# Performance work log

Hardware: AMD Instinct MI355X
Metric: run time of the kernel (lower is better)

The kernel has to match this reference:

```python
import jax, jax.numpy as jnp
import numpy as np

N_NODES = 50000
N_EDGES = 800000
N_GRAPHS = 256
IN_DIM, HIDDEN_DIM, EMBED_DIM = 128, 64, 128


def setup_inputs() -> dict:
    key = jax.random.key(0)
    ks = jax.random.split(key, 8)
    x = jax.random.normal(ks[0], (N_NODES, IN_DIM), dtype=jnp.float32)
    edge_index = jax.random.randint(ks[1], (2, N_EDGES), 0, N_NODES, dtype=jnp.int64)
    edge_weight = jax.random.uniform(ks[2], (N_EDGES,), dtype=jnp.float32)
    batch_vec = jnp.sort(jax.random.randint(ks[3], (N_NODES,), 0, N_GRAPHS, dtype=jnp.int64))
    # Glorot-ish params for the two GCNConv layers
    W1 = jax.random.normal(ks[4], (IN_DIM, HIDDEN_DIM), dtype=jnp.float32) / np.sqrt(IN_DIM)
    b1 = jnp.zeros((HIDDEN_DIM,), dtype=jnp.float32)
    W2 = jax.random.normal(ks[5], (HIDDEN_DIM, EMBED_DIM), dtype=jnp.float32) / np.sqrt(HIDDEN_DIM)
    b2 = jnp.zeros((EMBED_DIM,), dtype=jnp.float32)
    return {"x": x, "edge_index": edge_index, "edge_weight": edge_weight,
            "batch_vec": batch_vec, "W1": W1, "b1": b1, "W2": W2, "b2": b2}


def _gcn_conv(x, src, dst, ew, W, b, num_nodes):
    # PyG GCNConv: linear transform, add self-loops (weight 1), sym-normalize, aggregate at dst.
    h = x @ W  # [N, out]
    loops = jnp.arange(num_nodes, dtype=src.dtype)
    row = jnp.concatenate([src, loops])
    col = jnp.concatenate([dst, loops])
    w = jnp.concatenate([ew, jnp.ones((num_nodes,), x.dtype)])
    deg = jax.ops.segment_sum(w, col, num_segments=num_nodes)
    dis = jnp.where(deg > 0, jax.lax.rsqrt(deg), 0.0)  # deg^{-1/2}, inf -> 0
    norm = dis[row] * w * dis[col]  # [E+N]
    msg = h[row] * norm[:, None]  # gather + scale
    out = jax.ops.segment_sum(msg, col, num_segments=num_nodes)  # scatter-add
    return out + b


def reference(x, edge_index, edge_weight, batch_vec, W1, b1, W2, b2):
    src, dst = edge_index[0], edge_index[1]
    h = jax.nn.relu(_gcn_conv(x, src, dst, edge_weight, W1, b1, N_NODES))
    # dropout is identity at inference
    h = jax.nn.relu(_gcn_conv(h, src, dst, edge_weight, W2, b2, N_NODES))
    # global_mean_pool over graphs
    s = jax.ops.segment_sum(h, batch_vec, num_segments=N_GRAPHS)
    cnt = jax.ops.segment_sum(jnp.ones((N_NODES,), h.dtype), batch_vec, num_segments=N_GRAPHS)
    return s / jnp.maximum(cnt, 1.0)[:, None]
```

## Files before the change

### kernel.cpp

```cpp
#include <hip/hip_runtime.h>

constexpr int N_NODES  = 50000;
constexpr int N_EDGES  = 800000;
constexpr int N_GRAPHS = 256;
constexpr int IN_DIM   = 128;
constexpr int HID      = 64;
constexpr int EMB      = 128;
constexpr int NBKT     = 391;
constexpr int BCAP     = 4096;
constexpr int EB       = (N_EDGES + 1023) / 1024;
constexpr int GB       = (N_NODES + 31) / 32;
constexpr int GSB      = (N_NODES + 255) / 256;
constexpr int NB2      = 64;

constexpr size_t OFF_POOL = 0;
constexpr size_t OFF_GCUR = 32768;
constexpr size_t OFF_GST  = 33160;
constexpr size_t OFF_DIS  = 33424;
constexpr size_t OFF_RS   = 83424;
constexpr size_t OFF_REC  = 133424;
constexpr size_t OFF_PART = OFF_REC + 2 * (size_t)NBKT * BCAP;
constexpr size_t OFF_H1   = OFF_PART;
constexpr size_t OFF_H1P  = OFF_PART + 4 * (size_t)NBKT * BCAP;
constexpr size_t OFF_AGG2 = OFF_H1P;

__device__ inline unsigned bf16r(float f) {
    unsigned u = __float_as_uint(f);
    return (u + 0x7fffu + ((u >> 16) & 1u)) >> 16;
}
__device__ inline unsigned bf16pack2(float lo, float hi) {
    return bf16r(lo) | (bf16r(hi) << 16);
}
__device__ inline float bflo(unsigned v) { return __uint_as_float(v << 16); }
__device__ inline float bfhi(unsigned v) { return __uint_as_float(v & 0xffff0000u); }

__device__ inline void fma4(float4& acc, float s, const float4& v) {
    acc.x += s * v.x; acc.y += s * v.y; acc.z += s * v.z; acc.w += s * v.w;
}

__global__ __launch_bounds__(256) void k_p2(const int* __restrict__ src,
                                            const int* __restrict__ dst,
                                            const float* __restrict__ ew,
                                            int* __restrict__ gcur,
                                            uint4* __restrict__ part,
                                            const int* __restrict__ batch,
                                            int* __restrict__ gstart) {
    __shared__ int   lb[NBKT];
    __shared__ int   lc[NBKT];
    __shared__ int   es[1024];
    __shared__ int   ed[1024];
    __shared__ float ee[1024];
    int tid = threadIdx.x;
    if (blockIdx.x >= EB) {
        int i = (blockIdx.x - EB) * 256 + tid;
        if (i >= N_NODES) return;
        int g = batch[i];
        if (i == 0) {
            for (int gg = 0; gg <= g; ++gg) gstart[gg] = 0;
        } else {
            int gp = batch[i - 1];
            for (int gg = gp + 1; gg <= g; ++gg) gstart[gg] = i;
        }
        if (i == N_NODES - 1) {
            for (int gg = g + 1; gg <= N_GRAPHS; ++gg) gstart[gg] = N_NODES;
        }
        return;
    }
    for (int i = tid; i < NBKT; i += 256) lc[i] = 0;
    __syncthreads();
    int base = blockIdx.x * 1024;
    #pragma unroll
    for (int j = 0; j < 4; ++j) {
        int idx = j * 256 + tid;
        int e = base + idx;
        int d = 0, s = 0; float w = 0.f;
        if (e < N_EDGES) {
            d = dst[e]; s = src[e]; w = ew[e];
            atomicAdd(&lc[d >> 7], 1);
        }
        es[idx] = s; ed[idx] = d; ee[idx] = w;
    }
    __syncthreads();
    for (int i = tid; i < NBKT; i += 256) {
        int c = lc[i];
        lb[i] = c ? (i * BCAP + atomicAdd(&gcur[i], c)) : 0;
        lc[i] = 0;
    }
    __syncthreads();
    #pragma unroll
    for (int j = 0; j < 4; ++j) {
        int idx = j * 256 + tid;
        int e = base + idx;
        if (e < N_EDGES) {
            int d = ed[idx];
            int b = d >> 7;
            int r = atomicAdd(&lc[b], 1);
            part[lb[b] + r] = make_uint4((unsigned)es[idx], (unsigned)d,
                                         __float_as_uint(ee[idx]), 0u);
        }
    }
}

constexpr int SMEM_BYTES = 32768 + 32 * (IN_DIM + 4) * 4;
__global__ __launch_bounds__(256) void k_p3_gemm1(const uint4* __restrict__ part,
                                                  const int* __restrict__ gcur,
                                                  int* __restrict__ rs,
                                                  float* __restrict__ dis,
                                                  uint2* __restrict__ rec,
                                                  const float* __restrict__ x,
                                                  const float* __restrict__ W1,
                                                  unsigned* __restrict__ h) {
    __shared__ alignas(16) unsigned char smem[SMEM_BYTES];
    int tid = threadIdx.x;
    if (blockIdx.x < NBKT) {
        uint2* cache = (uint2*)smem;
        int*   cnt   = (int*)(smem + 32768);
        float* dgw   = (float*)(smem + 32768 + 512);
        int*   scn   = (int*)(smem + 32768 + 1024);
        int*   curx  = (int*)(smem + 32768 + 1536);
        int b = blockIdx.x;
        int ebeg = b * BCAP;
        int ne = gcur[b]; if (ne > BCAP) ne = BCAP;
        if (tid < 128) { cnt[tid] = 0; dgw[tid] = 0.f; }
        __syncthreads();
        for (int i = tid; i < ne; i += 256) {
            uint4 r = part[ebeg + i];
            int ld = (int)r.y & 127;
            cache[i] = make_uint2(r.x | ((unsigned)ld << 16), r.z);
            atomicAdd(&cnt[ld], 1);
            atomicAdd(&dgw[ld], __uint_as_float(r.z));
        }
        __syncthreads();
        int c = (tid < 128) ? cnt[tid] : 0;
        if (tid < 128) scn[tid] = c;
        __syncthreads();
        for (int off = 1; off < 128; off <<= 1) {
            int a = (tid >= off && tid < 128) ? scn[tid - off] : 0;
            __syncthreads();
            if (tid < 128) scn[tid] += a;
            __syncthreads();
        }
        if (tid < 128) {
            int node = (b << 7) + tid;
            if (node < N_NODES) {
                rs[node] = ebeg + scn[tid];
                dis[node] = rsqrtf(dgw[tid] + 1.0f);
            }
            curx[tid] = ebeg + scn[tid] - c;
        }
        __syncthreads();
        for (int i = tid; i < ne; i += 256) {
            uint2 q = cache[i];
            int ld = (int)(q.x >> 16);
            int pos = atomicAdd(&curx[ld], 1);
            rec[pos] = make_uint2(q.x & 0xFFFFu, q.y);
        }
        return;
    }
    float* Ws = (float*)smem;
    float (*xs)[IN_DIM + 4] = (float (*)[IN_DIM + 4])(smem + 32768);
    int bid = blockIdx.x - NBKT;
    const float4* W4 = (const float4*)W1;
    float4* Ws4 = (float4*)Ws;
    for (int i = tid; i < IN_DIM * HID / 4; i += 256) Ws4[i] = W4[i];
    int base = bid * 32;
    const float4* X4 = (const float4*)x;
    for (int i = tid; i < 32 * 32; i += 256) {
        int ln = i >> 5, kq = i & 31;
        int node = base + ln;
        float4 v = (node < N_NODES) ? X4[(size_t)node * 32 + kq]
                                    : make_float4(0.f, 0.f, 0.f, 0.f);
        *(float4*)&xs[ln][kq * 4] = v;
    }
    __syncthreads();
    int np = tid >> 4;
    int q  = tid & 15;
    int n0 = np * 2, n1 = n0 + 1;
    float4 a0 = make_float4(0.f, 0.f, 0.f, 0.f);
    float4 a1 = a0;
    #pragma unroll 4
    for (int k4 = 0; k4 < IN_DIM; k4 += 4) {
        float4 xv0 = *(const float4*)&xs[n0][k4];
        float4 xv1 = *(const float4*)&xs[n1][k4];
        float4 w0 = Ws4[(k4 + 0) * 16 + q];
        float4 w1 = Ws4[(k4 + 1) * 16 + q];
        float4 w2 = Ws4[(k4 + 2) * 16 + q];
        float4 w3 = Ws4[(k4 + 3) * 16 + q];
        fma4(a0, xv0.x, w0); fma4(a0, xv0.y, w1); fma4(a0, xv0.z, w2); fma4(a0, xv0.w, w3);
        fma4(a1, xv1.x, w0); fma4(a1, xv1.y, w1); fma4(a1, xv1.z, w2); fma4(a1, xv1.w, w3);
    }
    int nd0 = base + n0, nd1 = base + n1;
    if (nd0 < N_NODES) {
        uint2 p = make_uint2(bf16pack2(a0.x, a0.y), bf16pack2(a0.z, a0.w));
        ((uint2*)h)[(size_t)nd0 * 16 + q] = p;
    }
    if (nd1 < N_NODES) {
        uint2 p = make_uint2(bf16pack2(a1.x, a1.y), bf16pack2(a1.z, a1.w));
        ((uint2*)h)[(size_t)nd1 * 16 + q] = p;
    }
}

template <bool RELU_BIAS, bool OUT_BF16>
__global__ __launch_bounds__(256) void k_gather64(const uint2* __restrict__ rec,
                                                  const int* __restrict__ rs,
                                                  const float* __restrict__ dis,
                                                  const unsigned* __restrict__ T,
                                                  const float* __restrict__ bias,
                                                  void* __restrict__ outv) {
    int wave = (blockIdx.x * 256 + threadIdx.x) >> 6;
    if (wave >= N_NODES) return;
    int lane = threadIdx.x & 63;
    int grp  = lane >> 4;
    int l    = lane & 15;
    int n = wave;
    int begin = ((n & 127) == 0) ? ((n >> 7) * BCAP) : rs[n - 1];
    int end = rs[n];
    const uint2* T2 = (const uint2*)T;

    float a0 = 0.f, a1 = 0.f, a2 = 0.f, a3 = 0.f;
    float c0 = 0.f, c1 = 0.f, c2 = 0.f, c3 = 0.f;
    int k = begin + grp;
    while (k + 4 < end) {
        uint2 r0 = rec[k];
        uint2 r1 = rec[k + 4];
        float d0 = dis[r0.x];
        float d1 = dis[r1.x];
        uint2 t0 = T2[(size_t)r0.x * 16 + l];
        uint2 t1 = T2[(size_t)r1.x * 16 + l];
        float n0 = d0 * __uint_as_float(r0.y);
        float n1 = d1 * __uint_as_float(r1.y);
        a0 += bflo(t0.x) * n0; a1 += bfhi(t0.x) * n0;
        a2 += bflo(t0.y) * n0; a3 += bfhi(t0.y) * n0;
        c0 += bflo(t1.x) * n1; c1 += bfhi(t1.x) * n1;
        c2 += bflo(t1.y) * n1; c3 += bfhi(t1.y) * n1;
        k += 8;
    }
    if (k < end) {
        uint2 r = rec[k];
        float d = dis[r.x];
        uint2 t = T2[(size_t)r.x * 16 + l];
        float nn = d * __uint_as_float(r.y);
        a0 += bflo(t.x) * nn; a1 += bfhi(t.x) * nn;
        a2 += bflo(t.y) * nn; a3 += bfhi(t.y) * nn;
    }
    a0 += c0; a1 += c1; a2 += c2; a3 += c3;
    a0 += __shfl_xor(a0, 16, 64); a1 += __shfl_xor(a1, 16, 64);
    a2 += __shfl_xor(a2, 16, 64); a3 += __shfl_xor(a3, 16, 64);
    a0 += __shfl_xor(a0, 32, 64); a1 += __shfl_xor(a1, 32, 64);
    a2 += __shfl_xor(a2, 32, 64); a3 += __shfl_xor(a3, 32, 64);
    if (grp == 0) {
        float di = dis[n];
        uint2 t = T2[(size_t)n * 16 + l];
        a0 += bflo(t.x) * di; a1 += bfhi(t.x) * di;
        a2 += bflo(t.y) * di; a3 += bfhi(t.y) * di;
        a0 *= di; a1 *= di; a2 *= di; a3 *= di;
        if (RELU_BIAS) {
            float4 b = ((const float4*)bias)[l];
            a0 = fmaxf(a0 + b.x, 0.f);
            a1 = fmaxf(a1 + b.y, 0.f);
            a2 = fmaxf(a2 + b.z, 0.f);
            a3 = fmaxf(a3 + b.w, 0.f);
        }
        if (OUT_BF16) {
            ((uint2*)outv)[(size_t)n * 16 + l] =
                make_uint2(bf16pack2(a0, a1), bf16pack2(a2, a3));
        } else {
            ((float4*)outv)[(size_t)n * 16 + l] = make_float4(a0, a1, a2, a3);
        }
    }
}

__global__ __launch_bounds__(256) void k_gemm2_pool(const float* __restrict__ agg,
                                                    const float* __restrict__ W2,
                                                    const float* __restrict__ b2,
                                                    const int* __restrict__ batch,
                                                    float* __restrict__ pool) {
    __shared__ float Ws[HID * EMB];
    __shared__ float as[NB2][HID];
    __shared__ int   bs[NB2];
    int tid = threadIdx.x;
    const float4* W4 = (const float4*)W2;
    float4* Ws4 = (float4*)Ws;
    for (int i = tid; i < HID * EMB / 4; i += 256) Ws4[i] = W4[i];
    int base = blockIdx.x * NB2;
    const float4* A4 = (const float4*)agg;
    float4* as4 = (float4*)as;
    for (int i = tid; i < NB2 * HID / 4; i += 256) {
        int node = base + (i >> 4);
        as4[i] = (node < N_NODES) ? A4[(size_t)node * 16 + (i & 15)]
                                  : make_float4(0.f, 0.f, 0.f, 0.f);
    }
    if (tid < NB2) {
        int node = base + tid;
        bs[tid] = (node < N_NODES) ? batch[node] : -1;
    }
    __syncthreads();

    int c = tid & 31;
    int s = tid >> 5;
    int jc = c * 4;
    int nb = s * 8;
    float4 acc[8];
    #pragma unroll
    for (int i = 0; i < 8; ++i) acc[i] = make_float4(0.f, 0.f, 0.f, 0.f);
    #pragma unroll 4
    for (int k4 = 0; k4 < HID; k4 += 4) {
        float4 w0 = Ws4[(k4 + 0) * 32 + c];
        float4 w1 = Ws4[(k4 + 1) * 32 + c];
        float4 w2 = Ws4[(k4 + 2) * 32 + c];
        float4 w3 = Ws4[(k4 + 3) * 32 + c];
        #pragma unroll
        for (int i = 0; i < 8; ++i) {
            float4 av = *(const float4*)&as[nb + i][k4];
            fma4(acc[i], av.x, w0); fma4(acc[i], av.y, w1);
            fma4(acc[i], av.z, w2); fma4(acc[i], av.w, w3);
        }
    }
    float4 bq = *(const float4*)&b2[jc];
    float4 racc = make_float4(0.f, 0.f, 0.f, 0.f);
    int gcur = -1;
    #pragma unroll
    for (int i = 0; i < 8; ++i) {
        int g = bs[nb + i];
        if (g != gcur) {
            if (gcur >= 0) {
                float* p = &pool[(size_t)gcur * EMB + jc];
                atomicAdd(p + 0, racc.x); atomicAdd(p + 1, racc.y);
                atomicAdd(p + 2, racc.z); atomicAdd(p + 3, racc.w);
            }
            racc = make_float4(0.f, 0.f, 0.f, 0.f);
            gcur = g;
        }
        if (g < 0) continue;
        racc.x += fmaxf(acc[i].x + bq.x, 0.f);
        racc.y += fmaxf(acc[i].y + bq.y, 0.f);
        racc.z += fmaxf(acc[i].z + bq.z, 0.f);
        racc.w += fmaxf(acc[i].w + bq.w, 0.f);
    }
    if (gcur >= 0) {
        float* p = &pool[(size_t)gcur * EMB + jc];
        atomicAdd(p + 0, racc.x); atomicAdd(p + 1, racc.y);
        atomicAdd(p + 2, racc.z); atomicAdd(p + 3, racc.w);
    }
}

__global__ void k_divide(const float* __restrict__ pool, const int* __restrict__ gstart,
                         float* __restrict__ out) {
    int idx = blockIdx.x * blockDim.x + threadIdx.x;
    if (idx >= N_GRAPHS * EMB) return;
    int g = idx >> 7;
    float c = (float)(gstart[g + 1] - gstart[g]);
    out[idx] = pool[idx] / fmaxf(c, 1.0f);
}

extern "C" void kernel_launch(void* const* d_in, const int* in_sizes, int n_in,
                              void* d_out, int out_size, void* d_ws, size_t ws_size,
                              hipStream_t stream) {
    const float* x     = (const float*)d_in[0];
    const int*   eidx  = (const int*)d_in[1];
    const float* ew    = (const float*)d_in[2];
    const int*   batch = (const int*)d_in[3];
    const float* W1    = (const float*)d_in[4];
    const float* b1    = (const float*)d_in[5];
    const float* W2    = (const float*)d_in[6];
    const float* b2    = (const float*)d_in[7];
    float* out = (float*)d_out;

    const int* src = eidx;
    const int* dst = eidx + N_EDGES;

    float* ws     = (float*)d_ws;
    float* pool   = ws + OFF_POOL;
    int*   gcur   = (int*)(ws + OFF_GCUR);
    int*   gstart = (int*)(ws + OFF_GST);
    float* dis    = ws + OFF_DIS;
    int*   rs     = (int*)(ws + OFF_RS);
    uint2* rec    = (uint2*)(ws + OFF_REC);
    uint4* part   = (uint4*)(ws + OFF_PART);
    unsigned* h1  = (unsigned*)(ws + OFF_H1);
    unsigned* h1p = (unsigned*)(ws + OFF_H1P);
    float* agg2   = ws + OFF_AGG2;

    (void)hipMemsetAsync(pool, 0, (size_t)(32768 + NBKT) * sizeof(float), stream);

    k_p2<<<EB + GSB, 256, 0, stream>>>(src, dst, ew, gcur, part, batch, gstart);

    k_p3_gemm1<<<NBKT + GB, 256, 0, stream>>>(part, gcur, rs, dis, rec, x, W1, h1p);

    k_gather64<true, true><<<N_NODES / 4, 256, 0, stream>>>(rec, rs, dis, h1p, b1, h1);

    k_gather64<false, false><<<N_NODES / 4, 256, 0, stream>>>(rec, rs, dis, h1, nullptr, agg2);

    k_gemm2_pool<<<(N_NODES + NB2 - 1) / NB2, 256, 0, stream>>>(agg2, W2, b2, batch, pool);

    k_divide<<<(N_GRAPHS * EMB + 255) / 256, 256, 0, stream>>>(pool, gstart, out);
}
```

Baseline: 225.3 us.

## Fuse second-layer gather into GEMM2 and pooling kernel

```diff
diff --git a/kernel.cpp b/kernel.cpp
--- a/kernel.cpp
+++ b/kernel.cpp
@@ -22,7 +22,6 @@
 constexpr size_t OFF_PART = OFF_REC + 2 * (size_t)NBKT * BCAP;
 constexpr size_t OFF_H1   = OFF_PART;
 constexpr size_t OFF_H1P  = OFF_PART + 4 * (size_t)NBKT * BCAP;
-constexpr size_t OFF_AGG2 = OFF_H1P;
 
 __device__ inline unsigned bf16r(float f) {
     unsigned u = __float_as_uint(f);
@@ -200,13 +199,12 @@
     }
 }
 
-template <bool RELU_BIAS, bool OUT_BF16>
 __global__ __launch_bounds__(256) void k_gather64(const uint2* __restrict__ rec,
                                                   const int* __restrict__ rs,
                                                   const float* __restrict__ dis,
                                                   const unsigned* __restrict__ T,
                                                   const float* __restrict__ bias,
-                                                  void* __restrict__ outv) {
+                                                  unsigned* __restrict__ outv) {
     int wave = (blockIdx.x * 256 + threadIdx.x) >> 6;
     if (wave >= N_NODES) return;
     int lane = threadIdx.x & 63;
@@ -254,27 +252,21 @@
         a0 += bflo(t.x) * di; a1 += bfhi(t.x) * di;
         a2 += bflo(t.y) * di; a3 += bfhi(t.y) * di;
         a0 *= di; a1 *= di; a2 *= di; a3 *= di;
-        if (RELU_BIAS) {
-            float4 b = ((const float4*)bias)[l];
-            a0 = fmaxf(a0 + b.x, 0.f);
-            a1 = fmaxf(a1 + b.y, 0.f);
-            a2 = fmaxf(a2 + b.z, 0.f);
-            a3 = fmaxf(a3 + b.w, 0.f);
-        }
-        if (OUT_BF16) {
-            ((uint2*)outv)[(size_t)n * 16 + l] =
-                make_uint2(bf16pack2(a0, a1), bf16pack2(a2, a3));
-        } else {
-            ((float4*)outv)[(size_t)n * 16 + l] = make_float4(a0, a1, a2, a3);
-        }
-    }
-}
-
-__global__ __launch_bounds__(256) void k_gemm2_pool(const float* __restrict__ agg,
-                                                    const float* __restrict__ W2,
-                                                    const float* __restrict__ b2,
-                                                    const int* __restrict__ batch,
-                                                    float* __restrict__ pool) {
+        float4 b = ((const float4*)bias)[l];
+        a0 = fmaxf(a0 + b.x, 0.f);
+        a1 = fmaxf(a1 + b.y, 0.f);
+        a2 = fmaxf(a2 + b.z, 0.f);
+        a3 = fmaxf(a3 + b.w, 0.f);
+        ((uint2*)outv)[(size_t)n * 16 + l] =
+            make_uint2(bf16pack2(a0, a1), bf16pack2(a2, a3));
+    }
+}
+
+__global__ __launch_bounds__(256) void k_gather_gemm2_pool(
+        const uint2* __restrict__ rec, const int* __restrict__ rs,
+        const float* __restrict__ dis, const unsigned* __restrict__ T,
+        const float* __restrict__ W2, const float* __restrict__ b2,
+        const int* __restrict__ batch, float* __restrict__ pool) {
     __shared__ float Ws[HID * EMB];
     __shared__ float as[NB2][HID];
     __shared__ int   bs[NB2];
@@ -283,19 +275,65 @@
     float4* Ws4 = (float4*)Ws;
     for (int i = tid; i < HID * EMB / 4; i += 256) Ws4[i] = W4[i];
     int base = blockIdx.x * NB2;
-    const float4* A4 = (const float4*)agg;
-    float4* as4 = (float4*)as;
-    for (int i = tid; i < NB2 * HID / 4; i += 256) {
-        int node = base + (i >> 4);
-        as4[i] = (node < N_NODES) ? A4[(size_t)node * 16 + (i & 15)]
-                                  : make_float4(0.f, 0.f, 0.f, 0.f);
-    }
     if (tid < NB2) {
         int node = base + tid;
         bs[tid] = (node < N_NODES) ? batch[node] : -1;
     }
+    int lane = tid & 63;
+    int w    = tid >> 6;
+    int grp  = lane >> 4;
+    int l    = lane & 15;
+    const uint2* T2 = (const uint2*)T;
+    for (int j = 0; j < 16; ++j) {
+        int ln = w * 16 + j;
+        int n = base + ln;
+        if (n >= N_NODES) {
+            if (grp == 0) *(float4*)&as[ln][4 * l] = make_float4(0.f, 0.f, 0.f, 0.f);
+            continue;
+        }
+        int begin = ((n & 127) == 0) ? ((n >> 7) * BCAP) : rs[n - 1];
+        int end = rs[n];
+        float a0 = 0.f, a1 = 0.f, a2 = 0.f, a3 = 0.f;
+        float c0 = 0.f, c1 = 0.f, c2 = 0.f, c3 = 0.f;
+        int k = begin + grp;
+        while (k + 4 < end) {
+            uint2 r0 = rec[k];
+            uint2 r1 = rec[k + 4];
+            float d0 = dis[r0.x];
+            float d1 = dis[r1.x];
+            uint2 t0 = T2[(size_t)r0.x * 16 + l];
+            uint2 t1 = T2[(size_t)r1.x * 16 + l];
+            float n0 = d0 * __uint_as_float(r0.y);
+            float n1 = d1 * __uint_as_float(r1.y);
+            a0 += bflo(t0.x) * n0; a1 += bfhi(t0.x) * n0;
+            a2 += bflo(t0.y) * n0; a3 += bfhi(t0.y) * n0;
+            c0 += bflo(t1.x) * n1; c1 += bfhi(t1.x) * n1;
+            c2 += bflo(t1.y) * n1; c3 += bfhi(t1.y) * n1;
+            k += 8;
+        }
+        if (k < end) {
+            uint2 r = rec[k];
+            float d = dis[r.x];
+            uint2 t = T2[(size_t)r.x * 16 + l];
+            float nn = d * __uint_as_float(r.y);
+            a0 += bflo(t.x) * nn; a1 += bfhi(t.x) * nn;
+            a2 += bflo(t.y) * nn; a3 += bfhi(t.y) * nn;
+        }
+        a0 += c0; a1 += c1; a2 += c2; a3 += c3;
+        a0 += __shfl_xor(a0, 16, 64); a1 += __shfl_xor(a1, 16, 64);
+        a2 += __shfl_xor(a2, 16, 64); a3 += __shfl_xor(a3, 16, 64);
+        a0 += __shfl_xor(a0, 32, 64); a1 += __shfl_xor(a1, 32, 64);
+        a2 += __shfl_xor(a2, 32, 64); a3 += __shfl_xor(a3, 32, 64);
+        if (grp == 0) {
+            float di = dis[n];
+            uint2 t = T2[(size_t)n * 16 + l];
+            a0 += bflo(t.x) * di; a1 += bfhi(t.x) * di;
+            a2 += bflo(t.y) * di; a3 += bfhi(t.y) * di;
+            a0 *= di; a1 *= di; a2 *= di; a3 *= di;
+            *(float4*)&as[ln][4 * l] = make_float4(a0, a1, a2, a3);
+        }
+    }
     __syncthreads();
-
     int c = tid & 31;
     int s = tid >> 5;
     int jc = c * 4;
@@ -379,7 +417,6 @@
     uint4* part   = (uint4*)(ws + OFF_PART);
     unsigned* h1  = (unsigned*)(ws + OFF_H1);
     unsigned* h1p = (unsigned*)(ws + OFF_H1P);
-    float* agg2   = ws + OFF_AGG2;
 
     (void)hipMemsetAsync(pool, 0, (size_t)(32768 + NBKT) * sizeof(float), stream);
 
@@ -387,11 +424,10 @@
 
     k_p3_gemm1<<<NBKT + GB, 256, 0, stream>>>(part, gcur, rs, dis, rec, x, W1, h1p);
 
-    k_gather64<true, true><<<N_NODES / 4, 256, 0, stream>>>(rec, rs, dis, h1p, b1, h1);
-
-    k_gather64<false, false><<<N_NODES / 4, 256, 0, stream>>>(rec, rs, dis, h1, nullptr, agg2);
-
-    k_gemm2_pool<<<(N_NODES + NB2 - 1) / NB2, 256, 0, stream>>>(agg2, W2, b2, batch, pool);
+    k_gather64<<<N_NODES / 4, 256, 0, stream>>>(rec, rs, dis, h1p, b1, h1);
+
+    k_gather_gemm2_pool<<<(N_NODES + NB2 - 1) / NB2, 256, 0, stream>>>(
+        rec, rs, dis, h1, W2, b2, batch, pool);
 
     k_divide<<<(N_GRAPHS * EMB + 255) / 256, 256, 0, stream>>>(pool, gstart, out);
 }
```

After: 269.3 us. 1.2x slower.
